# Kernel optimization log

Hardware: AMD Instinct MI355X
Metric: run time of the kernel (lower is better)

## Reference

```python
import jax, jax.numpy as jnp
import numpy as np

N, D, H = 2048, 1024, 16
DH = D // H
SCALE = 1.0 / DH ** 0.5


def setup_inputs() -> dict:
    key = jax.random.key(0)
    k0, k1, k2 = jax.random.split(key, 3)
    lim_qkv = 1.0 / np.sqrt(D)
    lim_proj = 1.0 / np.sqrt(D)
    return {
        "x": jax.random.normal(k0, (N, D), dtype=jnp.float32),
        "w_qkv": jax.random.uniform(k1, (3 * D, D), jnp.float32, -lim_qkv, lim_qkv),
        "b_qkv": jnp.zeros((3 * D,), jnp.float32),
        "w_proj": jax.random.uniform(k2, (D, D), jnp.float32, -lim_proj, lim_proj),
        "b_proj": jnp.zeros((D,), jnp.float32),
    }


def reference(x, w_qkv, b_qkv, w_proj, b_proj) -> jnp.ndarray:
    # qkv linear: (N, D) -> (N, 3D)
    qkv = x @ w_qkv.T + b_qkv
    q, k, v = jnp.split(qkv, 3, axis=-1)
    # (N, D) -> (H, N, Dh)
    def _heads(a):
        return a.reshape(N, H, DH).transpose(1, 0, 2)
    q, k, v = map(_heads, (q, k, v))
    # full NxN scores per head (faithful to original einsum+softmax)
    attn = jax.nn.softmax(jnp.einsum('hnd,hmd->hnm', q * SCALE, k), axis=-1)
    out = jnp.einsum('hnm,hmd->hnd', attn, v)          # (H, N, Dh)
    out = out.transpose(1, 0, 2).reshape(N, D)
    return out @ w_proj.T + b_proj
```

## Files before the change

kernel.cpp:

```cpp
#include <hip/hip_runtime.h>
#include <hip/hip_bf16.h>
#include <cstdint>

typedef unsigned short u16;
typedef __attribute__((ext_vector_type(8)))  short bf16x8;
typedef __attribute__((ext_vector_type(4)))  float f32x4;
typedef __attribute__((ext_vector_type(16))) float f32x16;
typedef __attribute__((ext_vector_type(2)))  unsigned int uint2v;

#define N_TOK   2048
#define DMODEL  1024
#define NHEAD   16
#define DHEAD   64
#define QKV_N   3072
#define QK_LD   2048
#define NSPLIT  4
#define KV_PER  (N_TOK / NSPLIT)
#define C1_LOG2 0.1803368801111244f
#define M0_BASE 4.0f

__device__ __forceinline__ u16 f2b(float f) {
  uint32_t u = __float_as_uint(f);
  u += 0x7FFFu + ((u >> 16) & 1u);
  return (u16)(u >> 16);
}
__device__ __forceinline__ float b2f(u16 b) {
  return __uint_as_float(((uint32_t)b) << 16);
}
__device__ __forceinline__ float fexp2(float x) { return __builtin_amdgcn_exp2f(x); }

__device__ __forceinline__ uint32_t cvtpk(float lo, float hi) {
  uint32_t r;
  asm("v_cvt_pk_bf16_f32 %0, %1, %2" : "=v"(r) : "v"(lo), "v"(hi));
  return r;
}

__device__ __forceinline__ float xsum32(float x) {
  uint2v d = __builtin_amdgcn_permlane32_swap(__float_as_uint(x), __float_as_uint(x), false, false);
  return __uint_as_float(d.x) + __uint_as_float(d.y);
}

__device__ __forceinline__ void gload_lds16(const void* g, void* l) {
  __builtin_amdgcn_global_load_lds(
      (const __attribute__((address_space(1))) void*)g,
      (__attribute__((address_space(3))) void*)l,
      16, 0, 0);
}

__global__ __launch_bounds__(256)
void cvt_all(const float* __restrict__ x, const float* __restrict__ wq,
             const float* __restrict__ wp,
             u16* __restrict__ xb, u16* __restrict__ wqb, u16* __restrict__ wpb) {
  const int i = blockIdx.x * 256 + threadIdx.x;
  const int NX = (N_TOK * DMODEL) / 4;
  const int NQ = (3 * DMODEL * DMODEL) / 4;
  const float4* src; u16* dst; int j;
  if (i < NX)            { src = (const float4*)x;  dst = xb;  j = i; }
  else if (i < NX + NQ)  { src = (const float4*)wq; dst = wqb; j = i - NX; }
  else                   { src = (const float4*)wp; dst = wpb; j = i - NX - NQ; }
  const float4 v = src[j];
  ushort4 pk;
  pk.x = f2b(v.x); pk.y = f2b(v.y); pk.z = f2b(v.z); pk.w = f2b(v.w);
  ((ushort4*)dst)[j] = pk;
}

template<bool OUT_F32, bool FUSE_VT, int MI, int NI>
__global__ __launch_bounds__(256, 2)
void gemm_nt(const u16* __restrict__ A, const u16* __restrict__ B,
             const float* __restrict__ bias, void* __restrict__ Cv,
             u16* __restrict__ vtg, int ldc, int K) {
  __shared__ alignas(16) u16 As[2][MI * 32 * 64];
  __shared__ alignas(16) u16 Bs[2][NI * 32 * 64];
  const int tid = threadIdx.x;
  const int w = tid >> 6, l = tid & 63;
  const int lo = l & 15, hi = l >> 4;
  const int wr = w >> 1, wc = w & 1;
  const int bm = blockIdx.y * (MI * 32), bn = blockIdx.x * (NI * 32);
  f32x4 acc[MI][NI] = {};
  const int NK = K >> 6;

  auto stage = [&](int kb, int bufi) {
#pragma unroll
    for (int i = 0; i < MI; ++i) {
      const int c = w * (MI * 64) + i * 64 + l;
      const int r = c >> 3, gs = (c ^ r) & 7;
      gload_lds16(A + (size_t)(bm + r) * K + kb + gs * 8, (char*)As[bufi] + (size_t)c * 16);
    }
#pragma unroll
    for (int i = 0; i < NI; ++i) {
      const int c = w * (NI * 64) + i * 64 + l;
      const int r = c >> 3, gs = (c ^ r) & 7;
      gload_lds16(B + (size_t)(bn + r) * K + kb + gs * 8, (char*)Bs[bufi] + (size_t)c * 16);
    }
  };

  stage(0, 0);
  int buf = 0;
  for (int t = 0; t < NK; ++t) {
    if (t + 1 < NK) {
      stage((t + 1) * 64, buf ^ 1);
      if constexpr (MI + NI == 7)      asm volatile("s_waitcnt vmcnt(7)" ::: "memory");
      else if constexpr (MI + NI == 6) asm volatile("s_waitcnt vmcnt(6)" ::: "memory");
      else if constexpr (MI + NI == 4) asm volatile("s_waitcnt vmcnt(4)" ::: "memory");
      else                             asm volatile("s_waitcnt vmcnt(8)" ::: "memory");
    } else {
      asm volatile("s_waitcnt vmcnt(0)" ::: "memory");
    }
    __builtin_amdgcn_s_barrier();

    bf16x8 af[MI][2], bfr[NI][2];
#pragma unroll
    for (int mi = 0; mi < MI; ++mi)
#pragma unroll
      for (int ks = 0; ks < 2; ++ks) {
        const int ra = wr * (MI * 16) + mi * 16 + lo;
        af[mi][ks] = *(const bf16x8*)((const char*)As[buf] + ra * 128 +
                                      (((ks * 4 + hi) ^ (ra & 7)) << 4));
      }
#pragma unroll
    for (int ni = 0; ni < NI; ++ni)
#pragma unroll
      for (int ks = 0; ks < 2; ++ks) {
        const int rb = wc * (NI * 16) + ni * 16 + lo;
        bfr[ni][ks] = *(const bf16x8*)((const char*)Bs[buf] + rb * 128 +
                                       (((ks * 4 + hi) ^ (rb & 7)) << 4));
      }
#pragma unroll
    for (int mi = 0; mi < MI; ++mi)
#pragma unroll
      for (int ni = 0; ni < NI; ++ni)
#pragma unroll
        for (int ks = 0; ks < 2; ++ks)
          acc[mi][ni] = __builtin_amdgcn_mfma_f32_16x16x32_bf16(af[mi][ks], bfr[ni][ks], acc[mi][ni], 0, 0, 0);

    __builtin_amdgcn_s_barrier();
    buf ^= 1;
  }

#pragma unroll
  for (int mi = 0; mi < MI; ++mi)
#pragma unroll
    for (int ni = 0; ni < NI; ++ni) {
      const int col = bn + wc * (NI * 16) + ni * 16 + lo;
      const float bv = bias[col];
      if constexpr (FUSE_VT) {
        if (col >= 2 * DMODEL) {
          const int row0 = bm + wr * (MI * 16) + mi * 16 + hi * 4;
          ushort4 pk;
          pk.x = f2b(acc[mi][ni][0] + bv);
          pk.y = f2b(acc[mi][ni][1] + bv);
          pk.z = f2b(acc[mi][ni][2] + bv);
          pk.w = f2b(acc[mi][ni][3] + bv);
          *(ushort4*)(vtg + (size_t)(col - 2 * DMODEL) * N_TOK + row0) = pk;
        } else {
          const float sc = (col < DMODEL) ? C1_LOG2 : 1.0f;
#pragma unroll
          for (int j = 0; j < 4; ++j) {
            const int row = bm + wr * (MI * 16) + mi * 16 + hi * 4 + j;
            ((u16*)Cv)[(size_t)row * QK_LD + col] = f2b((acc[mi][ni][j] + bv) * sc);
          }
        }
      } else {
#pragma unroll
        for (int j = 0; j < 4; ++j) {
          const int row = bm + wr * (MI * 16) + mi * 16 + hi * 4 + j;
          const float v = acc[mi][ni][j] + bv;
          if constexpr (OUT_F32) ((float*)Cv)[(size_t)row * ldc + col] = v;
          else                   ((u16*)Cv)[(size_t)row * ldc + col] = f2b(v);
        }
      }
    }
}

#define FRAG(BASE, ROW, SLOT) \
  (*(const bf16x8*)((const char*)(BASE) + (ROW) * 128 + ((((SLOT) ^ ((ROW) & 7))) << 4)))

#define SOFTPACK(SA, SB, PFR, LS) do {                                          \
    float tsum_ = 0.f;                                                          \
    _Pragma("unroll")                                                           \
    for (int ks = 0; ks < 4; ++ks) {                                            \
      float q_[8];                                                              \
      _Pragma("unroll")                                                         \
      for (int j = 0; j < 8; ++j) {                                             \
        const int idx = (ks & 1) * 8 + j;                                       \
        q_[j] = fexp2(((ks < 2) ? (SA)[idx] : (SB)[idx]) - M0_BASE);            \
      }                                                                         \
      tsum_ += ((q_[0] + q_[1]) + (q_[2] + q_[3])) + ((q_[4] + q_[5]) + (q_[6] + q_[7])); \
      uint32_t a1 = cvtpk(q_[0], q_[1]);                                        \
      uint32_t a2 = cvtpk(q_[2], q_[3]);                                        \
      uint32_t b1 = cvtpk(q_[4], q_[5]);                                        \
      uint32_t b2 = cvtpk(q_[6], q_[7]);                                        \
      uint2v r1 = __builtin_amdgcn_permlane32_swap(a1, b1, false, false);       \
      uint2v r2 = __builtin_amdgcn_permlane32_swap(a2, b2, false, false);       \
      union { uint32_t u[4]; bf16x8 h; } cv_;                                   \
      cv_.u[0] = r1.x; cv_.u[1] = r2.x; cv_.u[2] = r1.y; cv_.u[3] = r2.y;       \
      (PFR)[ks] = cv_.h;                                                        \
    }                                                                           \
    (LS) += tsum_;                                                              \
  } while (0)

__global__ __launch_bounds__(256, 2)
void attn3(const u16* __restrict__ qkb, const u16* __restrict__ vtg,
           u16* __restrict__ PO, float* __restrict__ lbuf) {
  __shared__ alignas(16) u16 SMEM[4][64 * 64];
  const int tid = threadIdx.x;
  const int w = tid >> 6, l = tid & 63;
  const int lo = l & 31, hi = l >> 5;

  int bid = (int)blockIdx.x;
  bid = (bid & 7) * 64 + (bid >> 3);
  const int h  = bid >> 5;
  const int qb = (bid >> 2) & 7;
  const int z  = bid & 3;
  const int q0w = qb * 256 + w * 64;
  const int kv0 = z * KV_PER;

  bf16x8 qf0[4], qf1[4];
  {
    const u16* qs0 = qkb + (size_t)(q0w + lo) * QK_LD + h * 64 + hi * 8;
    const u16* qs1 = qkb + (size_t)(q0w + 32 + lo) * QK_LD + h * 64 + hi * 8;
#pragma unroll
    for (int ds = 0; ds < 4; ++ds) { qf0[ds] = *(const bf16x8*)(qs0 + ds * 16);
                                     qf1[ds] = *(const bf16x8*)(qs1 + ds * 16); }
  }

  f32x16 o0 = {}, o1 = {}, o2 = {}, o3 = {};
  float lsum0 = 0.f, lsum1 = 0.f;

#define STAGE(KB, B) do {                                                       \
    _Pragma("unroll")                                                           \
    for (int i_ = 0; i_ < 2; ++i_) {                                            \
      const int c_ = w * 128 + i_ * 64 + l;                                     \
      const int r_ = c_ >> 3;                                                   \
      const int gs_ = (c_ ^ r_) & 7;                                            \
      gload_lds16(qkb + (size_t)((KB) + r_) * QK_LD + DMODEL + h * 64 + gs_ * 8,\
                  (char*)SMEM[B] + (size_t)(w * 128 + i_ * 64) * 16);           \
      gload_lds16(vtg + (size_t)(h * 64 + r_) * N_TOK + (KB) + gs_ * 8,         \
                  (char*)SMEM[2 + (B)] + (size_t)(w * 128 + i_ * 64) * 16);     \
    }                                                                           \
  } while (0)

  STAGE(kv0, 0);
  int buf = 0;
  for (int t = 0; t < KV_PER / 64; ++t) {
    if (t + 1 < KV_PER / 64) {
      STAGE(kv0 + (t + 1) * 64, buf ^ 1);
      asm volatile("s_waitcnt vmcnt(4)" ::: "memory");
    } else {
      asm volatile("s_waitcnt vmcnt(0)" ::: "memory");
    }
    __builtin_amdgcn_s_barrier();

    const u16* Kb = SMEM[buf];
    const u16* Vb = SMEM[2 + buf];

    f32x16 s0 = {}, s1 = {}, s2 = {}, s3 = {};
    __builtin_amdgcn_s_setprio(1);
#pragma unroll
    for (int ds = 0; ds < 4; ++ds) {
      bf16x8 k0 = FRAG(Kb, lo, ds * 2 + hi);
      bf16x8 k1 = FRAG(Kb, 32 + lo, ds * 2 + hi);
      s0 = __builtin_amdgcn_mfma_f32_32x32x16_bf16(k0, qf0[ds], s0, 0, 0, 0);
      s1 = __builtin_amdgcn_mfma_f32_32x32x16_bf16(k1, qf0[ds], s1, 0, 0, 0);
      s2 = __builtin_amdgcn_mfma_f32_32x32x16_bf16(k0, qf1[ds], s2, 0, 0, 0);
      s3 = __builtin_amdgcn_mfma_f32_32x32x16_bf16(k1, qf1[ds], s3, 0, 0, 0);
    }
    __builtin_amdgcn_s_setprio(0);

    bf16x8 pfr0[4], pfr1[4];
    SOFTPACK(s0, s1, pfr0, lsum0);
    SOFTPACK(s2, s3, pfr1, lsum1);

    __builtin_amdgcn_s_setprio(1);
#pragma unroll
    for (int ks = 0; ks < 4; ++ks) {
      bf16x8 v0 = FRAG(Vb, lo, ks * 2 + hi);
      bf16x8 v1 = FRAG(Vb, 32 + lo, ks * 2 + hi);
      o0 = __builtin_amdgcn_mfma_f32_32x32x16_bf16(v0, pfr0[ks], o0, 0, 0, 0);
      o1 = __builtin_amdgcn_mfma_f32_32x32x16_bf16(v1, pfr0[ks], o1, 0, 0, 0);
      o2 = __builtin_amdgcn_mfma_f32_32x32x16_bf16(v0, pfr1[ks], o2, 0, 0, 0);
      o3 = __builtin_amdgcn_mfma_f32_32x32x16_bf16(v1, pfr1[ks], o3, 0, 0, 0);
    }
    __builtin_amdgcn_s_setprio(0);

    __builtin_amdgcn_s_barrier();
    buf ^= 1;
  }
#undef STAGE

  lsum0 = xsum32(lsum0);
  lsum1 = xsum32(lsum1);

  u16* Ow = ((u16*)SMEM) + w * 4096;
  const float inv0 = 1.0f / lsum0;
  const float inv1 = 1.0f / lsum1;
#pragma unroll
  for (int r = 0; r < 16; ++r) {
    const int crow = (r & 3) + 8 * (r >> 2) + 4 * hi;
    const int c0 = crow, c1 = 32 + crow;
    const int s0i = ((c0 >> 3) ^ (lo & 7)) << 3, s1i = ((c1 >> 3) ^ (lo & 7)) << 3;
    Ow[lo * 64 + s0i + (c0 & 7)] = f2b(o0[r] * inv0);
    Ow[lo * 64 + s1i + (c1 & 7)] = f2b(o1[r] * inv0);
    Ow[(32 + lo) * 64 + s0i + (c0 & 7)] = f2b(o2[r] * inv1);
    Ow[(32 + lo) * 64 + s1i + (c1 & 7)] = f2b(o3[r] * inv1);
  }
  if (hi == 0) {
    lbuf[((size_t)z * NHEAD + h) * N_TOK + q0w + lo] = lsum0;
    lbuf[((size_t)z * NHEAD + h) * N_TOK + q0w + 32 + lo] = lsum1;
  }
  asm volatile("s_waitcnt lgkmcnt(0)" ::: "memory");
  __builtin_amdgcn_sched_barrier(0);
  u16* pobase = PO + (((size_t)z * NHEAD + h) * N_TOK + q0w) * DHEAD;
#pragma unroll
  for (int i = 0; i < 8; ++i) {
    const int c = i * 64 + l;
    const int rr = c >> 3, sl = c & 7;
    bf16x8 v = *(const bf16x8*)(Ow + rr * 64 + sl * 8);
    const int cs = sl ^ (rr & 7);
    *(bf16x8*)(pobase + (size_t)rr * DHEAD + cs * 8) = v;
  }
}

__global__ __launch_bounds__(256)
void combine(const u16* __restrict__ PO, const float* __restrict__ lbuf,
             u16* __restrict__ attb) {
  const int idx = blockIdx.x * 256 + threadIdx.x;
  const int row = idx >> 3;
  const int c8  = (idx & 7) * 8;
  const int h = row >> 11;
  const int q = row & (N_TOK - 1);

  float wsum = 0.f, acc8[8] = {};
#pragma unroll
  for (int zz = 0; zz < NSPLIT; ++zz) {
    const float wz = lbuf[((size_t)zz * NHEAD + h) * N_TOK + q];
    wsum += wz;
    bf16x8 po = *(const bf16x8*)(PO + (((size_t)zz * NHEAD + h) * N_TOK + q) * DHEAD + c8);
#pragma unroll
    for (int j = 0; j < 8; ++j) acc8[j] += wz * b2f((u16)po[j]);
  }
  const float invw = 1.0f / wsum;
  union { u16 s[8]; bf16x8 h8; } ov;
#pragma unroll
  for (int j = 0; j < 8; ++j) ov.s[j] = f2b(acc8[j] * invw);
  *(bf16x8*)(attb + (size_t)q * DMODEL + h * 64 + c8) = ov.h8;
}

extern "C" void kernel_launch(void* const* d_in, const int* in_sizes, int n_in,
                              void* d_out, int out_size, void* d_ws, size_t ws_size,
                              hipStream_t stream) {
  const float* x      = (const float*)d_in[0];
  const float* w_qkv  = (const float*)d_in[1];
  const float* b_qkv  = (const float*)d_in[2];
  const float* w_proj = (const float*)d_in[3];
  const float* b_proj = (const float*)d_in[4];
  float* out = (float*)d_out;

  char* ws = (char*)d_ws;
  u16*    xb     = (u16*)(ws + (0u  << 20));
  u16*    wqkvb  = (u16*)(ws + (8u  << 20));
  u16*    wprojb = (u16*)(ws + (16u << 20));
  u16*    qkb    = (u16*)(ws + (24u << 20));
  u16*    vtg    = (u16*)(ws + (40u << 20));
  u16*    PO     = (u16*)(ws + (48u << 20));
  float*  lbuf   = (float*)(ws + (64u << 20));
  u16*    attb   = (u16*)(ws + (66u << 20));
  if (ws_size < (80u << 20)) return;

  cvt_all<<<6144, 256, 0, stream>>>(x, w_qkv, w_proj, xb, wqkvb, wprojb);

  gemm_nt<false, true, 4, 3><<<dim3(QKV_N / 96, N_TOK / 128), 256, 0, stream>>>(
      xb, wqkvb, b_qkv, (void*)qkb, vtg, QK_LD, DMODEL);

  attn3<<<8 * NHEAD * NSPLIT, 256, 0, stream>>>(qkb, vtg, PO, lbuf);

  combine<<<(N_TOK * NHEAD * 8) / 256, 256, 0, stream>>>(PO, lbuf, attb);

  gemm_nt<true, false, 2, 2><<<dim3(DMODEL / 64, N_TOK / 64), 256, 0, stream>>>(
      attb, wprojb, b_proj, (void*)out, nullptr, DMODEL, DMODEL);
}
```

Baseline: 73.70 us.

## Fuse split-KV combine into attention via last-block atomic counter election

Removes the separate combine kernel launch. Each attention block bumps an atomic counter per (head, query-block) after writing its partial output, and the last of the NSPLIT blocks merges the partials into attb. The counters are zeroed inside the conversion kernel. This saves one launch and its tail, but the merge now runs on only one of four blocks per tile, which serialises some work and adds fences and atomics.

```diff
diff --git a/kernel.cpp b/kernel.cpp
--- a/kernel.cpp
+++ b/kernel.cpp
@@ -50,8 +50,10 @@
 __global__ __launch_bounds__(256)
 void cvt_all(const float* __restrict__ x, const float* __restrict__ wq,
              const float* __restrict__ wp,
-             u16* __restrict__ xb, u16* __restrict__ wqb, u16* __restrict__ wpb) {
+             u16* __restrict__ xb, u16* __restrict__ wqb, u16* __restrict__ wpb,
+             int* __restrict__ cnt) {
   const int i = blockIdx.x * 256 + threadIdx.x;
+  if (i < NHEAD * 8) cnt[i] = 0;
   const int NX = (N_TOK * DMODEL) / 4;
   const int NQ = (3 * DMODEL * DMODEL) / 4;
   const float4* src; u16* dst; int j;
@@ -201,8 +203,10 @@
 
 __global__ __launch_bounds__(256, 2)
 void attn3(const u16* __restrict__ qkb, const u16* __restrict__ vtg,
-           u16* __restrict__ PO, float* __restrict__ lbuf) {
+           u16* __restrict__ PO, float* __restrict__ lbuf,
+           u16* __restrict__ attb, int* __restrict__ cnt) {
   __shared__ alignas(16) u16 SMEM[4][64 * 64];
+  __shared__ int elect;
   const int tid = threadIdx.x;
   const int w = tid >> 6, l = tid & 63;
   const int lo = l & 31, hi = l >> 5;
@@ -319,31 +323,35 @@
     const int cs = sl ^ (rr & 7);
     *(bf16x8*)(pobase + (size_t)rr * DHEAD + cs * 8) = v;
   }
-}
-
-__global__ __launch_bounds__(256)
-void combine(const u16* __restrict__ PO, const float* __restrict__ lbuf,
-             u16* __restrict__ attb) {
-  const int idx = blockIdx.x * 256 + threadIdx.x;
-  const int row = idx >> 3;
-  const int c8  = (idx & 7) * 8;
-  const int h = row >> 11;
-  const int q = row & (N_TOK - 1);
-
-  float wsum = 0.f, acc8[8] = {};
-#pragma unroll
-  for (int zz = 0; zz < NSPLIT; ++zz) {
-    const float wz = lbuf[((size_t)zz * NHEAD + h) * N_TOK + q];
-    wsum += wz;
-    bf16x8 po = *(const bf16x8*)(PO + (((size_t)zz * NHEAD + h) * N_TOK + q) * DHEAD + c8);
-#pragma unroll
-    for (int j = 0; j < 8; ++j) acc8[j] += wz * b2f((u16)po[j]);
-  }
-  const float invw = 1.0f / wsum;
-  union { u16 s[8]; bf16x8 h8; } ov;
-#pragma unroll
-  for (int j = 0; j < 8; ++j) ov.s[j] = f2b(acc8[j] * invw);
-  *(bf16x8*)(attb + (size_t)q * DMODEL + h * 64 + c8) = ov.h8;
+
+  __threadfence();
+  __syncthreads();
+  if (tid == 0) elect = (atomicAdd(&cnt[h * 8 + qb], 1) == NSPLIT - 1);
+  __syncthreads();
+  if (elect) {
+    __threadfence();
+#pragma unroll
+    for (int it = 0; it < 8; ++it) {
+      const int idx = it * 256 + tid;
+      const int row = idx >> 3;
+      const int c8  = (idx & 7) * 8;
+      const int q = qb * 256 + row;
+      float wsum = 0.f, a8[8] = {};
+#pragma unroll
+      for (int zz = 0; zz < NSPLIT; ++zz) {
+        const float wz = lbuf[((size_t)zz * NHEAD + h) * N_TOK + q];
+        wsum += wz;
+        bf16x8 po = *(const bf16x8*)(PO + (((size_t)zz * NHEAD + h) * N_TOK + q) * DHEAD + c8);
+#pragma unroll
+        for (int j = 0; j < 8; ++j) a8[j] += wz * b2f((u16)po[j]);
+      }
+      const float invw = 1.0f / wsum;
+      union { u16 s[8]; bf16x8 h8; } ov;
+#pragma unroll
+      for (int j = 0; j < 8; ++j) ov.s[j] = f2b(a8[j] * invw);
+      *(bf16x8*)(attb + (size_t)q * DMODEL + h * 64 + c8) = ov.h8;
+    }
+  }
 }
 
 extern "C" void kernel_launch(void* const* d_in, const int* in_sizes, int n_in,
@@ -365,16 +373,15 @@
   u16*    PO     = (u16*)(ws + (48u << 20));
   float*  lbuf   = (float*)(ws + (64u << 20));
   u16*    attb   = (u16*)(ws + (66u << 20));
+  int*    cnt    = (int*)(ws + (71u << 20));
   if (ws_size < (80u << 20)) return;
 
-  cvt_all<<<6144, 256, 0, stream>>>(x, w_qkv, w_proj, xb, wqkvb, wprojb);
+  cvt_all<<<6144, 256, 0, stream>>>(x, w_qkv, w_proj, xb, wqkvb, wprojb, cnt);
 
   gemm_nt<false, true, 4, 3><<<dim3(QKV_N / 96, N_TOK / 128), 256, 0, stream>>>(
       xb, wqkvb, b_qkv, (void*)qkb, vtg, QK_LD, DMODEL);
 
-  attn3<<<8 * NHEAD * NSPLIT, 256, 0, stream>>>(qkb, vtg, PO, lbuf);
-
-  combine<<<(N_TOK * NHEAD * 8) / 256, 256, 0, stream>>>(PO, lbuf, attb);
+  attn3<<<8 * NHEAD * NSPLIT, 256, 0, stream>>>(qkb, vtg, PO, lbuf, attb, cnt);
 
   gemm_nt<true, false, 2, 2><<<dim3(DMODEL / 64, N_TOK / 64), 256, 0, stream>>>(
       attb, wprojb, b_proj, (void*)out, nullptr, DMODEL, DMODEL);
```

Result: slower. 140.4 us (+90.5%).
